# Kernel tuning notes

Measured on AMD Instinct MI355X. Metric: run time of the kernel, lower is better.

Reference implementation:

```python
import jax, jax.numpy as jnp
import numpy as np

B, H, S, D = 8, 16, 1024, 128
DROP_P = 0.1


def setup_inputs() -> dict:
    key = jax.random.key(0)
    kq, kk, kv, ks = jax.random.split(key, 4)
    q = jax.random.normal(kq, (B, H, S, D), dtype=jnp.float32)
    k = jax.random.normal(kk, (B, H, S, D), dtype=jnp.float32)
    v = jax.random.normal(kv, (B, H, S, D), dtype=jnp.float32)
    # avoid near-zero divisors: uniform in [0.5, 1.5)
    inv_scale_factor = jax.random.uniform(ks, (1, 1, 1, S), dtype=jnp.float32,
                                          minval=0.5, maxval=1.5)
    return {"q": q, "k": k, "v": v, "inv_scale_factor": inv_scale_factor}


def reference(q, k, v, inv_scale_factor):
    # scores: [B, H, Sq, Sk]
    scores = jnp.einsum('bhqd,bhkd->bhqk', q, k)
    scaled = scores / inv_scale_factor  # broadcast over score columns
    probs = jax.nn.softmax(scaled, axis=-1)
    # dropout p=0.1 (train mode), deterministic key, inverted scaling
    keep = jax.random.bernoulli(jax.random.key(42), 1.0 - DROP_P, probs.shape)
    dropped = jnp.where(keep, probs / (1.0 - DROP_P), 0.0)
    return jnp.einsum('bhqk,bhkd->bhqd', dropped, v)
```

## Files before the change

kernel.cpp:

```cpp
#include <hip/hip_runtime.h>
#include <hip/hip_bf16.h>
#include <stdint.h>

#define SS 1024
#define DD 128
#define TQ 64
#define TK 64
#define NKT (SS/TK)
#define THREADS 256
#define NBLK (128 * (SS/TQ))
#define NHEAD 128
#define LOG2E 1.44269504088896340736f
#define DEFER_THR 11.5415603f

#define TILE_SHORTS 16384
#define PREP_BYTES ((size_t)NHEAD * NKT * TILE_SHORTS * 2)

typedef _Float16 f16x8 __attribute__((ext_vector_type(8)));
typedef _Float16 f16x4 __attribute__((ext_vector_type(4)));
typedef short bf16x8 __attribute__((ext_vector_type(8)));
typedef float f32x4  __attribute__((ext_vector_type(4)));

__device__ __forceinline__ uint32_t rotl32(uint32_t v, uint32_t s) {
  return __builtin_amdgcn_alignbit(v, v, 32u - s);
}
__device__ __forceinline__ uint32_t threefry_bits(uint32_t ctr) {
  const uint32_t K0 = 0u, K1 = 42u;
  const uint32_t K2 = K0 ^ K1 ^ 0x1BD11BDAu;
  uint32_t x0 = K0;
  uint32_t x1 = ctr + K1;
#define TF_RND(r) { x0 += x1; x1 = rotl32(x1, r); x1 ^= x0; }
  TF_RND(13u) TF_RND(15u) TF_RND(26u) TF_RND(6u)
  x0 += K1; x1 += K2 + 1u;
  TF_RND(17u) TF_RND(29u) TF_RND(16u) TF_RND(24u)
  x0 += K2; x1 += K0 + 2u;
  TF_RND(13u) TF_RND(15u) TF_RND(26u) TF_RND(6u)
  x0 += K0; x1 += K1 + 3u;
  TF_RND(17u) TF_RND(29u) TF_RND(16u) TF_RND(24u)
  x0 += K1; x1 += K2 + 4u;
  TF_RND(13u) TF_RND(15u) TF_RND(26u) TF_RND(6u)
  x0 += K2; x1 += K0 + 5u;
#undef TF_RND
  return x0 ^ x1;
}
__device__ __forceinline__ uint32_t maskhalf(uint32_t base) {
  uint32_t h = 0u;
#pragma unroll 4
  for (int b = 0; b < 16; ++b)
    h |= (threefry_bits(base + (uint32_t)b) < 0xE6666600u) ? (1u << b) : 0u;
  return h;
}

__device__ __forceinline__ short f2bf(float x) {
  return __builtin_bit_cast(short, __float2bfloat16(x));
}
__device__ __forceinline__ float bf2f(short b) {
  return __uint_as_float(((uint32_t)(uint16_t)b) << 16);
}
__device__ __forceinline__ uint32_t pack2(short a, short b) {
  return (uint32_t)(uint16_t)a | ((uint32_t)(uint16_t)b << 16);
}
__device__ __forceinline__ void split2(float x, short& hi, short& lo) {
  hi = f2bf(x);
  lo = f2bf(x - bf2f(hi));
}

#define MFMA16F(A, B, C) __builtin_amdgcn_mfma_f32_16x16x32_f16(A, B, C, 0, 0, 0)
#define MFMA16B(A, B, C) __builtin_amdgcn_mfma_f32_16x16x32_bf16(A, B, C, 0, 0, 0)

__device__ __forceinline__ void gl_lds16(const void* g, void* lds) {
  auto gp = (const __attribute__((address_space(1))) uint32_t*)(uintptr_t)g;
  auto lp = (__attribute__((address_space(3))) uint32_t*)(uintptr_t)lds;
  __builtin_amdgcn_global_load_lds(gp, lp, 16, 0, 0);
}

__global__ __launch_bounds__(256) void pm_prep(
    const float* __restrict__ Kg, const float* __restrict__ Vg,
    const float* __restrict__ isf, short* __restrict__ prep)
{
  __shared__ short lv[64 * 132];
  const int bid = blockIdx.x;
  const int head = bid >> 4, kt = bid & 15;
  const int tid = threadIdx.x;
  const float* Kt  = Kg + ((size_t)head * SS + (size_t)kt * TK) * DD;
  const float* Vtg = Vg + ((size_t)head * SS + (size_t)kt * TK) * DD;
  short* tile = prep + (size_t)bid * TILE_SHORTS;

#pragma unroll
  for (int i = 0; i < 8; ++i) {
    int f = tid * 4 + i * 1024;
    int k = f >> 7, d = f & 127;
    float rsk = LOG2E * __builtin_amdgcn_rcpf(isf[kt * TK + k]);
    float4 k4 = *(const float4*)(Kt + f);
    f16x4 kh = { (_Float16)(k4.x * rsk), (_Float16)(k4.y * rsk),
                 (_Float16)(k4.z * rsk), (_Float16)(k4.w * rsk) };
    int idx = k * 128 + (d & 7) + 8 * ((d >> 3) ^ (k & 15));
    *(f16x4*)&tile[idx] = kh;
    float4 v4 = *(const float4*)(Vtg + f);
    f16x4 vh = { (_Float16)v4.x, (_Float16)v4.y, (_Float16)v4.z, (_Float16)v4.w };
    *(f16x4*)&lv[k * 132 + d] = vh;
  }
  __syncthreads();
#pragma unroll
  for (int j = 0; j < 4; ++j) {
    int c = tid * 4 + j;
    int d = c >> 3, s = c & 7;
    int kk0 = (s ^ (d & 7)) * 8;
    short tmp[8];
#pragma unroll
    for (int e = 0; e < 8; ++e) tmp[e] = lv[(kk0 + e) * 132 + d];
    *(uint4*)&tile[8192 + d * 64 + s * 8] = *(uint4*)tmp;
  }
}

#define SMEM_SHORTS 21504

__global__ __launch_bounds__(THREADS) void pm_attn(
    const float* __restrict__ Qg, const short* __restrict__ prep,
    float* __restrict__ Og)
{
  __shared__ __align__(16) short smem[SMEM_SHORTS];
  short* const Kfs = smem;
  short* const Vts = smem + 8192;
  short* const Pt  = smem + 16384;
  unsigned short* const Ms = (unsigned short*)(smem + 20992);

  const int tid  = threadIdx.x;
  const int lane = tid & 63;
  const int wid  = tid >> 6;
  const int lg   = lane >> 4;
  const int tx   = lane & 15;

  const int swz   = (blockIdx.x & 7) * (NBLK / 8) + (blockIdx.x >> 3);
  const int head  = swz >> 4;
  const int qbase = (swz & 15) * TQ;

  const size_t hoff = (size_t)head * (SS * DD);
  const float* Qh = Qg + hoff + (size_t)qbase * DD;
  float*       Oh = Og + hoff + (size_t)qbase * DD;

  const int qrow = wid * 16 + tx;
  f16x8 qf[4];
#pragma unroll
  for (int ds = 0; ds < 4; ++ds) {
    const float* qp = Qh + qrow * DD + ds * 32 + lg * 8;
    float x[8];
    *(float4*)&x[0] = *(const float4*)qp;
    *(float4*)&x[4] = *(const float4*)(qp + 4);
#pragma unroll
    for (int e = 0; e < 8; ++e) qf[ds][e] = (_Float16)x[e];
  }

  f32x4 acc[8];
#pragma unroll
  for (int n = 0; n < 8; ++n) acc[n] = (f32x4){0.f, 0.f, 0.f, 0.f};
  float mrun = -1e30f, lrun = 0.f;

  const uint32_t ctrbase = ((uint32_t)head << 20) |
                           ((uint32_t)(qbase + (tid >> 2)) << 10) |
                           (uint32_t)((tid & 3) * 16);
  Ms[tid]       = (unsigned short)maskhalf(ctrbase);
  Ms[256 + tid] = (unsigned short)maskhalf(ctrbase + 64u);

  const int vswz = tx & 7;

  for (int kt = 0; kt < NKT; ++kt) {
    __syncthreads();

    {
      const char* gw = (const char*)(prep + (size_t)(head * NKT + kt) * TILE_SHORTS)
                       + wid * 8192 + lane * 16;
      char* lw = (char*)smem + wid * 8192;
#pragma unroll
      for (int i = 0; i < 8; ++i)
        gl_lds16(gw + i * 1024, lw + i * 1024);
    }

    uint32_t nexth = 0;
    if (kt + 2 < NKT) nexth = maskhalf(ctrbase + (uint32_t)((kt + 2) * 64));

    __syncthreads();

    f32x4 sc[4];
#pragma unroll
    for (int kj = 0; kj < 4; ++kj) sc[kj] = (f32x4){0.f, 0.f, 0.f, 0.f};
#pragma unroll
    for (int ds = 0; ds < 4; ++ds) {
#pragma unroll
      for (int kj = 0; kj < 4; ++kj) {
        int off = (kj * 16 + tx) * 128 + 8 * ((ds * 4 + lg) ^ tx);
        f16x8 kf = *(const f16x8*)&Kfs[off];
        sc[kj] = MFMA16F(kf, qf[ds], sc[kj]);
      }
    }

    float pmax = sc[0][0];
#pragma unroll
    for (int kj = 0; kj < 4; ++kj)
#pragma unroll
      for (int r = 0; r < 4; ++r) pmax = fmaxf(pmax, sc[kj][r]);

    if (!__all(pmax <= mrun + DEFER_THR)) {
      float mt = fmaxf(pmax, __shfl_xor(pmax, 16, 64));
      mt = fmaxf(mt, __shfl_xor(mt, 32, 64));
      float mnew = fmaxf(mrun, mt);
      float corr = exp2f(mrun - mnew);
      lrun *= corr;
#pragma unroll
      for (int r = 0; r < 4; ++r) {
        float cr = __shfl(corr, (lane & 48) | (lg * 4 + r), 64);
#pragma unroll
        for (int n = 0; n < 8; ++n) acc[n][r] *= cr;
      }
      mrun = mnew;
    }

    uint2 ww = *(const uint2*)&Ms[(kt & 1) * 256 + (wid * 16 + tx) * 4];
    float rsum = 0.f;
#pragma unroll
    for (int kj = 0; kj < 4; ++kj) {
      uint32_t w = (kj < 2) ? ww.x : ww.y;
      int bb = (kj & 1) * 16 + lg * 4;
      float p0 = exp2f(sc[kj][0] - mrun);
      float p1 = exp2f(sc[kj][1] - mrun);
      float p2 = exp2f(sc[kj][2] - mrun);
      float p3 = exp2f(sc[kj][3] - mrun);
      rsum += (p0 + p1) + (p2 + p3);
      f16x4 ph;
      ph[0] = ((w >> (bb + 0)) & 1u) ? (_Float16)p0 : (_Float16)0.f;
      ph[1] = ((w >> (bb + 1)) & 1u) ? (_Float16)p1 : (_Float16)0.f;
      ph[2] = ((w >> (bb + 2)) & 1u) ? (_Float16)p2 : (_Float16)0.f;
      ph[3] = ((w >> (bb + 3)) & 1u) ? (_Float16)p3 : (_Float16)0.f;
      *(f16x4*)&Pt[(wid * 16 + tx) * 72 + kj * 16 + lg * 4] = ph;
    }
    rsum += __shfl_xor(rsum, 16, 64);
    rsum += __shfl_xor(rsum, 32, 64);
    lrun += rsum;

    __syncthreads();

    if (kt + 2 < NKT) Ms[(kt & 1) * 256 + tid] = (unsigned short)nexth;

#pragma unroll
    for (int ks = 0; ks < 2; ++ks) {
      f16x8 pa = *(const f16x8*)&Pt[(wid * 16 + tx) * 72 + ks * 32 + lg * 8];
#pragma unroll
      for (int n = 0; n < 8; ++n) {
        int dr = n * 16 + tx;
        f16x8 vb = *(const f16x8*)&Vts[dr * 64 + 8 * ((ks * 4 + lg) ^ vswz)];
        acc[n] = MFMA16F(pa, vb, acc[n]);
      }
    }
  }

#pragma unroll
  for (int r = 0; r < 4; ++r) {
    float lr = __shfl(lrun, (lane & 48) | (lg * 4 + r), 64);
    float inv = 1.0f / (0.9f * lr);
    int orow = wid * 16 + lg * 4 + r;
#pragma unroll
    for (int n = 0; n < 8; ++n)
      Oh[orow * DD + n * 16 + tx] = acc[n][r] * inv;
  }
}

#define THREADS_FB 512
#define SMEM_SHORTS_FB 36864
__global__ __launch_bounds__(THREADS_FB) void pm_attn_fb(
    const float* __restrict__ Qg, const float* __restrict__ Kg,
    const float* __restrict__ Vg, const float* __restrict__ isf,
    float* __restrict__ Og)
{
  __shared__ __align__(16) short smem[SMEM_SHORTS_FB];
  short* const Khi = smem;
  short* const Klo = smem + 8704;
  short* const Vt  = smem + 17408;
  short* const Pts = smem + 26624;
  unsigned short* const Ms = (unsigned short*)(smem + 35840);

  const int tid  = threadIdx.x;
  const int lane = tid & 63;
  const int wid  = tid >> 6;
  const int lg   = lane >> 4;
  const int tx   = lane & 15;

  const int swz   = (blockIdx.x & 7) * 128 + (blockIdx.x >> 3);
  const int head  = swz >> 3;
  const int qbase = (swz & 7) * 128;

  const size_t hoff = (size_t)head * (SS * DD);
  const float* Qh = Qg + hoff + (size_t)qbase * DD;
  const float* Kh = Kg + hoff;
  const float* Vh = Vg + hoff;
  float*       Oh = Og + hoff + (size_t)qbase * DD;

  const int qrow = wid * 16 + tx;
  bf16x8 qhi[4], qlo[4];
#pragma unroll
  for (int ds = 0; ds < 4; ++ds) {
    const float* qp = Qh + qrow * DD + ds * 32 + lg * 8;
    float x[8];
    *(float4*)&x[0] = *(const float4*)qp;
    *(float4*)&x[4] = *(const float4*)(qp + 4);
#pragma unroll
    for (int e = 0; e < 8; ++e) {
      short h, l;
      split2(x[e], h, l);
      qhi[ds][e] = h;
      qlo[ds][e] = l;
    }
  }

  f32x4 acc[8];
#pragma unroll
  for (int n = 0; n < 8; ++n) acc[n] = (f32x4){0.f, 0.f, 0.f, 0.f};
  float mrun = -1e30f, lrun = 0.f;

  const uint32_t ctrbase = ((uint32_t)head << 20) |
                           ((uint32_t)(qbase + (tid >> 2)) << 10) |
                           (uint32_t)((tid & 3) * 16);
  Ms[tid]       = (unsigned short)maskhalf(ctrbase);
  Ms[512 + tid] = (unsigned short)maskhalf(ctrbase + 64u);

  const int vd = tid & 127;
  const int vq = tid >> 7;

  for (int kt = 0; kt < NKT; ++kt) {
    const float* Kt  = Kh + (size_t)kt * (TK * DD);
    const float* Vtg = Vh + (size_t)kt * (TK * DD);

    __syncthreads();
#pragma unroll
    for (int i = 0; i < 4; ++i) {
      int f = tid * 4 + i * 2048;
      int row = f >> 7, col = f & 127;
      float rsk = LOG2E * __builtin_amdgcn_rcpf(isf[kt * 64 + row]);
      float4 k4 = *(const float4*)(Kt + f);
      short h0, h1, h2, h3, l0, l1, l2, l3;
      split2(k4.x * rsk, h0, l0); split2(k4.y * rsk, h1, l1);
      split2(k4.z * rsk, h2, l2); split2(k4.w * rsk, h3, l3);
      *(uint2*)&Khi[row * 136 + col] = (uint2){pack2(h0, h1), pack2(h2, h3)};
      *(uint2*)&Klo[row * 136 + col] = (uint2){pack2(l0, l1), pack2(l2, l3)};
    }
#pragma unroll
    for (int j4 = 0; j4 < 4; ++j4) {
      int k0 = vq * 16 + j4 * 4;
      float a0 = Vtg[(k0 + 0) * DD + vd];
      float a1 = Vtg[(k0 + 1) * DD + vd];
      float a2 = Vtg[(k0 + 2) * DD + vd];
      float a3 = Vtg[(k0 + 3) * DD + vd];
      *(uint2*)&Vt[vd * 72 + k0] =
          (uint2){pack2(f2bf(a0), f2bf(a1)), pack2(f2bf(a2), f2bf(a3))};
    }
    __syncthreads();

    f32x4 sc[4];
#pragma unroll
    for (int kj = 0; kj < 4; ++kj) sc[kj] = (f32x4){0.f, 0.f, 0.f, 0.f};
#pragma unroll
    for (int ds = 0; ds < 4; ++ds) {
#pragma unroll
      for (int kj = 0; kj < 4; ++kj) {
        int off = (kj * 16 + tx) * 136 + ds * 32 + lg * 8;
        bf16x8 bhi = *(const bf16x8*)&Khi[off];
        bf16x8 blo = *(const bf16x8*)&Klo[off];
        sc[kj] = MFMA16B(bhi, qhi[ds], sc[kj]);
        sc[kj] = MFMA16B(bhi, qlo[ds], sc[kj]);
        sc[kj] = MFMA16B(blo, qhi[ds], sc[kj]);
      }
    }

    float pmax = sc[0][0];
#pragma unroll
    for (int kj = 0; kj < 4; ++kj)
#pragma unroll
      for (int r = 0; r < 4; ++r) pmax = fmaxf(pmax, sc[kj][r]);

    if (!__all(pmax <= mrun + DEFER_THR)) {
      float mt = fmaxf(pmax, __shfl_xor(pmax, 16, 64));
      mt = fmaxf(mt, __shfl_xor(mt, 32, 64));
      float mnew = fmaxf(mrun, mt);
      float corr = exp2f(mrun - mnew);
      lrun *= corr;
#pragma unroll
      for (int r = 0; r < 4; ++r) {
        float cr = __shfl(corr, (lane & 48) | (lg * 4 + r), 64);
#pragma unroll
        for (int n = 0; n < 8; ++n) acc[n][r] *= cr;
      }
      mrun = mnew;
    }

    uint2 ww = *(const uint2*)&Ms[(kt & 1) * 512 + (wid * 16 + tx) * 4];
    float rsum = 0.f;
#pragma unroll
    for (int kj = 0; kj < 4; ++kj) {
      uint32_t w = (kj < 2) ? ww.x : ww.y;
      int bb = (kj & 1) * 16 + lg * 4;
      float p0 = exp2f(sc[kj][0] - mrun);
      float p1 = exp2f(sc[kj][1] - mrun);
      float p2 = exp2f(sc[kj][2] - mrun);
      float p3 = exp2f(sc[kj][3] - mrun);
      rsum += (p0 + p1) + (p2 + p3);
      short b0 = ((w >> (bb + 0)) & 1u) ? f2bf(p0) : (short)0;
      short b1 = ((w >> (bb + 1)) & 1u) ? f2bf(p1) : (short)0;
      short b2 = ((w >> (bb + 2)) & 1u) ? f2bf(p2) : (short)0;
      short b3 = ((w >> (bb + 3)) & 1u) ? f2bf(p3) : (short)0;
      *(uint2*)&Pts[(wid * 16 + tx) * 72 + kj * 16 + lg * 4] =
          (uint2){pack2(b0, b1), pack2(b2, b3)};
    }
    rsum += __shfl_xor(rsum, 16, 64);
    rsum += __shfl_xor(rsum, 32, 64);
    lrun += rsum;

    uint32_t nexth = 0;
    if (kt + 2 < NKT) nexth = maskhalf(ctrbase + (uint32_t)((kt + 2) * 64));

    __syncthreads();

    if (kt + 2 < NKT) Ms[(kt & 1) * 512 + tid] = (unsigned short)nexth;

#pragma unroll
    for (int ks = 0; ks < 2; ++ks) {
      bf16x8 pa = *(const bf16x8*)&Pts[(wid * 16 + tx) * 72 + ks * 32 + lg * 8];
#pragma unroll
      for (int n = 0; n < 8; ++n) {
        bf16x8 vb = *(const bf16x8*)&Vt[(n * 16 + tx) * 72 + ks * 32 + lg * 8];
        acc[n] = MFMA16B(pa, vb, acc[n]);
      }
    }
  }

#pragma unroll
  for (int r = 0; r < 4; ++r) {
    float lr = __shfl(lrun, (lane & 48) | (lg * 4 + r), 64);
    float inv = 1.0f / (0.9f * lr);
    int orow = wid * 16 + lg * 4 + r;
#pragma unroll
    for (int n = 0; n < 8; ++n)
      Oh[orow * DD + n * 16 + tx] = acc[n][r] * inv;
  }
}

extern "C" void kernel_launch(void* const* d_in, const int* in_sizes, int n_in,
                              void* d_out, int out_size, void* d_ws, size_t ws_size,
                              hipStream_t stream) {
  const float* q   = (const float*)d_in[0];
  const float* k   = (const float*)d_in[1];
  const float* v   = (const float*)d_in[2];
  const float* isf = (const float*)d_in[3];

  if (ws_size >= PREP_BYTES) {
    pm_prep<<<dim3(NHEAD * NKT), dim3(256), 0, stream>>>(k, v, isf, (short*)d_ws);
    pm_attn<<<dim3(NBLK), dim3(THREADS), 0, stream>>>(
        q, (const short*)d_ws, (float*)d_out);
  } else {
    pm_attn_fb<<<dim3(NHEAD * 8), dim3(THREADS_FB), 0, stream>>>(
        q, k, v, isf, (float*)d_out);
  }
}
```

Measured before the change: 365.7 us.

## Keep P in registers for PV via 16x16x16 MFMA, drop LDS P round-trip

```diff
diff --git a/kernel.cpp b/kernel.cpp
--- a/kernel.cpp
+++ b/kernel.cpp
@@ -14,7 +14,8 @@
 #define DEFER_THR 11.5415603f
 
 #define TILE_SHORTS 16384
-#define PREP_BYTES ((size_t)NHEAD * NKT * TILE_SHORTS * 2)
+#define TILE_BYTES  32768
+#define PREP_BYTES ((size_t)NHEAD * NKT * TILE_BYTES)
 
 typedef _Float16 f16x8 __attribute__((ext_vector_type(8)));
 typedef _Float16 f16x4 __attribute__((ext_vector_type(4)));
@@ -64,9 +65,14 @@
   hi = f2bf(x);
   lo = f2bf(x - bf2f(hi));
 }
-
-#define MFMA16F(A, B, C) __builtin_amdgcn_mfma_f32_16x16x32_f16(A, B, C, 0, 0, 0)
+__device__ __forceinline__ uint32_t pkrtz(float a, float b) {
+  return __builtin_bit_cast(uint32_t, __builtin_amdgcn_cvt_pkrtz(a, b));
+}
+
+#define MFMA_QK(A, B, C) __builtin_amdgcn_mfma_f32_16x16x32_f16(A, B, C, 0, 0, 0)
+#define MFMA_PV(A, B, C) __builtin_amdgcn_mfma_f32_16x16x16f16(A, B, C, 0, 0, 0)
 #define MFMA16B(A, B, C) __builtin_amdgcn_mfma_f32_16x16x32_bf16(A, B, C, 0, 0, 0)
+#define EXP2(x) __builtin_amdgcn_exp2f(x)
 
 __device__ __forceinline__ void gl_lds16(const void* g, void* lds) {
   auto gp = (const __attribute__((address_space(1))) uint32_t*)(uintptr_t)g;
@@ -101,29 +107,29 @@
     *(f16x4*)&lv[k * 132 + d] = vh;
   }
   __syncthreads();
-#pragma unroll
-  for (int j = 0; j < 4; ++j) {
-    int c = tid * 4 + j;
-    int d = c >> 3, s = c & 7;
-    int kk0 = (s ^ (d & 7)) * 8;
-    short tmp[8];
-#pragma unroll
-    for (int e = 0; e < 8; ++e) tmp[e] = lv[(kk0 + e) * 132 + d];
-    *(uint4*)&tile[8192 + d * 64 + s * 8] = *(uint4*)tmp;
-  }
-}
-
-#define SMEM_SHORTS 21504
-
-__global__ __launch_bounds__(THREADS) void pm_attn(
+  {
+    int d = tid >> 1;
+    int s0 = (tid & 1) * 8;
+#pragma unroll
+    for (int j = 0; j < 8; ++j) {
+      int s = s0 + j;
+      int k0 = (s ^ (d & 15)) * 4;
+      short tmp[4];
+#pragma unroll
+      for (int e = 0; e < 4; ++e) tmp[e] = lv[(k0 + e) * 132 + d];
+      *(uint2*)&tile[8192 + d * 64 + s * 4] = *(uint2*)tmp;
+    }
+  }
+}
+
+#define SMEM_SHORTS 16896
+
+__global__ __launch_bounds__(THREADS, 4) void pm_attn(
     const float* __restrict__ Qg, const short* __restrict__ prep,
     float* __restrict__ Og)
 {
   __shared__ __align__(16) short smem[SMEM_SHORTS];
-  short* const Kfs = smem;
-  short* const Vts = smem + 8192;
-  short* const Pt  = smem + 16384;
-  unsigned short* const Ms = (unsigned short*)(smem + 20992);
+  unsigned short* const Ms = (unsigned short*)(smem + 16384);
 
   const int tid  = threadIdx.x;
   const int lane = tid & 63;
@@ -151,33 +157,45 @@
     for (int e = 0; e < 8; ++e) qf[ds][e] = (_Float16)x[e];
   }
 
+  const short* kb[4];
+#pragma unroll
+  for (int ds = 0; ds < 4; ++ds)
+    kb[ds] = &smem[tx * 128 + (((ds * 4 + lg) ^ tx) << 3)];
+  const short* vb[4];
+#pragma unroll
+  for (int kj = 0; kj < 4; ++kj)
+    vb[kj] = &smem[8192 + tx * 64 + (((kj * 4 + lg) ^ tx) << 2)];
+
   f32x4 acc[8];
 #pragma unroll
   for (int n = 0; n < 8; ++n) acc[n] = (f32x4){0.f, 0.f, 0.f, 0.f};
-  float mrun = -1e30f, lrun = 0.f;
+  float mrun = -1e30f, lpart = 0.f;
 
   const uint32_t ctrbase = ((uint32_t)head << 20) |
                            ((uint32_t)(qbase + (tid >> 2)) << 10) |
                            (uint32_t)((tid & 3) * 16);
   Ms[tid]       = (unsigned short)maskhalf(ctrbase);
   Ms[256 + tid] = (unsigned short)maskhalf(ctrbase + 64u);
-
-  const int vswz = tx & 7;
+  uint32_t pending = 0;
+
+  const char* gsrc0 = (const char*)prep + (size_t)(head * NKT) * TILE_BYTES
+                      + wid * 1024 + lane * 16;
+  char* const ldst0 = (char*)smem + wid * 1024;
 
   for (int kt = 0; kt < NKT; ++kt) {
     __syncthreads();
 
+    if (kt >= 1 && kt + 1 < NKT)
+      Ms[((kt + 1) & 1) * 256 + tid] = (unsigned short)pending;
+
     {
-      const char* gw = (const char*)(prep + (size_t)(head * NKT + kt) * TILE_SHORTS)
-                       + wid * 8192 + lane * 16;
-      char* lw = (char*)smem + wid * 8192;
+      const char* gs = gsrc0 + (size_t)kt * TILE_BYTES;
 #pragma unroll
       for (int i = 0; i < 8; ++i)
-        gl_lds16(gw + i * 1024, lw + i * 1024);
-    }
-
-    uint32_t nexth = 0;
-    if (kt + 2 < NKT) nexth = maskhalf(ctrbase + (uint32_t)((kt + 2) * 64));
+        gl_lds16(gs + i * 4096, ldst0 + i * 4096);
+    }
+
+    if (kt + 2 < NKT) pending = maskhalf(ctrbase + (uint32_t)((kt + 2) * 64));
 
     __syncthreads();
 
@@ -186,11 +204,11 @@
     for (int kj = 0; kj < 4; ++kj) sc[kj] = (f32x4){0.f, 0.f, 0.f, 0.f};
 #pragma unroll
     for (int ds = 0; ds < 4; ++ds) {
+      f16x8 qv = qf[ds];
 #pragma unroll
       for (int kj = 0; kj < 4; ++kj) {
-        int off = (kj * 16 + tx) * 128 + 8 * ((ds * 4 + lg) ^ tx);
-        f16x8 kf = *(const f16x8*)&Kfs[off];
-        sc[kj] = MFMA16F(kf, qf[ds], sc[kj]);
+        f16x8 kf = *(const f16x8*)(kb[ds] + kj * 2048);
+        sc[kj] = MFMA_QK(kf, qv, sc[kj]);
       }
     }
 
@@ -204,8 +222,8 @@
       float mt = fmaxf(pmax, __shfl_xor(pmax, 16, 64));
       mt = fmaxf(mt, __shfl_xor(mt, 32, 64));
       float mnew = fmaxf(mrun, mt);
-      float corr = exp2f(mrun - mnew);
-      lrun *= corr;
+      float corr = EXP2(mrun - mnew);
+      lpart *= corr;
 #pragma unroll
       for (int r = 0; r < 4; ++r) {
         float cr = __shfl(corr, (lane & 48) | (lg * 4 + r), 64);
@@ -216,46 +234,34 @@
     }
 
     uint2 ww = *(const uint2*)&Ms[(kt & 1) * 256 + (wid * 16 + tx) * 4];
-    float rsum = 0.f;
 #pragma unroll
     for (int kj = 0; kj < 4; ++kj) {
-      uint32_t w = (kj < 2) ? ww.x : ww.y;
+      uint32_t wbits = (kj & 2) ? ww.y : ww.x;
       int bb = (kj & 1) * 16 + lg * 4;
-      float p0 = exp2f(sc[kj][0] - mrun);
-      float p1 = exp2f(sc[kj][1] - mrun);
-      float p2 = exp2f(sc[kj][2] - mrun);
-      float p3 = exp2f(sc[kj][3] - mrun);
-      rsum += (p0 + p1) + (p2 + p3);
-      f16x4 ph;
-      ph[0] = ((w >> (bb + 0)) & 1u) ? (_Float16)p0 : (_Float16)0.f;
-      ph[1] = ((w >> (bb + 1)) & 1u) ? (_Float16)p1 : (_Float16)0.f;
-      ph[2] = ((w >> (bb + 2)) & 1u) ? (_Float16)p2 : (_Float16)0.f;
-      ph[3] = ((w >> (bb + 3)) & 1u) ? (_Float16)p3 : (_Float16)0.f;
-      *(f16x4*)&Pt[(wid * 16 + tx) * 72 + kj * 16 + lg * 4] = ph;
-    }
-    rsum += __shfl_xor(rsum, 16, 64);
-    rsum += __shfl_xor(rsum, 32, 64);
-    lrun += rsum;
-
-    __syncthreads();
-
-    if (kt + 2 < NKT) Ms[(kt & 1) * 256 + tid] = (unsigned short)nexth;
-
-#pragma unroll
-    for (int ks = 0; ks < 2; ++ks) {
-      f16x8 pa = *(const f16x8*)&Pt[(wid * 16 + tx) * 72 + ks * 32 + lg * 8];
+      float p0 = EXP2(sc[kj][0] - mrun);
+      float p1 = EXP2(sc[kj][1] - mrun);
+      float p2 = EXP2(sc[kj][2] - mrun);
+      float p3 = EXP2(sc[kj][3] - mrun);
+      lpart += (p0 + p1) + (p2 + p3);
+      float m0 = ((wbits >> (bb + 0)) & 1u) ? p0 : 0.f;
+      float m1 = ((wbits >> (bb + 1)) & 1u) ? p1 : 0.f;
+      float m2 = ((wbits >> (bb + 2)) & 1u) ? p2 : 0.f;
+      float m3 = ((wbits >> (bb + 3)) & 1u) ? p3 : 0.f;
+      uint2 pu = { pkrtz(m0, m1), pkrtz(m2, m3) };
+      f16x4 pa = __builtin_bit_cast(f16x4, pu);
 #pragma unroll
       for (int n = 0; n < 8; ++n) {
-        int dr = n * 16 + tx;
-        f16x8 vb = *(const f16x8*)&Vts[dr * 64 + 8 * ((ks * 4 + lg) ^ vswz)];
-        acc[n] = MFMA16F(pa, vb, acc[n]);
-      }
-    }
-  }
-
+        f16x4 vv = *(const f16x4*)(vb[kj] + n * 1024);
+        acc[n] = MFMA_PV(pa, vv, acc[n]);
+      }
+    }
+  }
+
+  lpart += __shfl_xor(lpart, 16, 64);
+  lpart += __shfl_xor(lpart, 32, 64);
 #pragma unroll
   for (int r = 0; r < 4; ++r) {
-    float lr = __shfl(lrun, (lane & 48) | (lg * 4 + r), 64);
+    float lr = __shfl(lpart, (lane & 48) | (lg * 4 + r), 64);
     float inv = 1.0f / (0.9f * lr);
     int orow = wid * 16 + lg * 4 + r;
 #pragma unroll
@@ -380,7 +386,7 @@
       float mt = fmaxf(pmax, __shfl_xor(pmax, 16, 64));
       mt = fmaxf(mt, __shfl_xor(mt, 32, 64));
       float mnew = fmaxf(mrun, mt);
-      float corr = exp2f(mrun - mnew);
+      float corr = EXP2(mrun - mnew);
       lrun *= corr;
 #pragma unroll
       for (int r = 0; r < 4; ++r) {
@@ -397,10 +403,10 @@
     for (int kj = 0; kj < 4; ++kj) {
       uint32_t w = (kj < 2) ? ww.x : ww.y;
       int bb = (kj & 1) * 16 + lg * 4;
-      float p0 = exp2f(sc[kj][0] - mrun);
-      float p1 = exp2f(sc[kj][1] - mrun);
-      float p2 = exp2f(sc[kj][2] - mrun);
-      float p3 = exp2f(sc[kj][3] - mrun);
+      float p0 = EXP2(sc[kj][0] - mrun);
+      float p1 = EXP2(sc[kj][1] - mrun);
+      float p2 = EXP2(sc[kj][2] - mrun);
+      float p3 = EXP2(sc[kj][3] - mrun);
       rsum += (p0 + p1) + (p2 + p3);
       short b0 = ((w >> (bb + 0)) & 1u) ? f2bf(p0) : (short)0;
       short b1 = ((w >> (bb + 1)) & 1u) ? f2bf(p1) : (short)0;
@@ -425,8 +431,8 @@
       bf16x8 pa = *(const bf16x8*)&Pts[(wid * 16 + tx) * 72 + ks * 32 + lg * 8];
 #pragma unroll
       for (int n = 0; n < 8; ++n) {
-        bf16x8 vb = *(const bf16x8*)&Vt[(n * 16 + tx) * 72 + ks * 32 + lg * 8];
-        acc[n] = MFMA16B(pa, vb, acc[n]);
+        bf16x8 vbv = *(const bf16x8*)&Vt[(n * 16 + tx) * 72 + ks * 32 + lg * 8];
+        acc[n] = MFMA16B(pa, vbv, acc[n]);
       }
     }
   }
```

Result: faster. 348.1 us (-4.8%).
